# Kernel optimization log

Measured on AMD Instinct MI355X. Metric: run time of the kernel, lower is better.

## Reference

```python
import jax, jax.numpy as jnp
import numpy as np

D_IN = 4096
NUM_HEADS = 32
NUM_KV_GROUPS = 8
HEAD_DIM = D_IN // NUM_HEADS  # 128 (init overwrites head_dim)
GROUP_SIZE = NUM_HEADS // NUM_KV_GROUPS
SEQ = 2048
BATCH = 1
EPS = 1e-6


def layernorm(t, w, b):
    mu = jnp.mean(t, axis=-1, keepdims=True)
    var = jnp.var(t, axis=-1, keepdims=True)
    return (t - mu) * jax.lax.rsqrt(var + EPS) * w + b


def rope(t, cos, sin):
    # t: [B, H, S, D]; cos/sin: [S, D] broadcast over B, H
    half = t.shape[-1] // 2
    x1, x2 = t[..., :half], t[..., half:]
    rot = jnp.concatenate([-x2, x1], axis=-1)
    return t * cos + rot * sin


def setup_inputs() -> dict:
    key = jax.random.key(0)
    ks = jax.random.split(key, 10)
    x = jax.random.normal(ks[0], (BATCH, SEQ, D_IN), dtype=jnp.float32)
    mask = jnp.triu(jnp.ones((SEQ, SEQ), dtype=bool), k=1)  # True = masked (causal)
    # RoPE tables
    inv_freq = 1.0 / (10000.0 ** (np.arange(0, HEAD_DIM, 2, dtype=np.float32) / HEAD_DIM))
    pos = np.arange(SEQ, dtype=np.float32)
    ang = np.einsum('s,d->sd', pos, inv_freq)  # [S, D/2]
    ang = np.concatenate([ang, ang], axis=-1)  # [S, D]
    cos = jnp.asarray(np.cos(ang))
    sin = jnp.asarray(np.sin(ang))
    s = 0.02
    Wq = jax.random.normal(ks[1], (D_IN, NUM_HEADS * HEAD_DIM), dtype=jnp.float32) * s
    Wk = jax.random.normal(ks[2], (D_IN, NUM_KV_GROUPS * HEAD_DIM), dtype=jnp.float32) * s
    Wv = jax.random.normal(ks[3], (D_IN, NUM_KV_GROUPS * HEAD_DIM), dtype=jnp.float32) * s
    Wo = jax.random.normal(ks[4], (NUM_HEADS * HEAD_DIM, D_IN), dtype=jnp.float32) * s
    qn_w = jnp.ones((HEAD_DIM,), jnp.float32)
    qn_b = jnp.zeros((HEAD_DIM,), jnp.float32)
    kn_w = jnp.ones((HEAD_DIM,), jnp.float32)
    kn_b = jnp.zeros((HEAD_DIM,), jnp.float32)
    return {"x": x, "mask": mask, "cos": cos, "sin": sin, "Wq": Wq, "Wk": Wk,
            "Wv": Wv, "Wo": Wo, "qn_w": qn_w, "qn_b": qn_b, "kn_w": kn_w, "kn_b": kn_b}


def reference(x, mask, cos, sin, Wq, Wk, Wv, Wo, qn_w, qn_b, kn_w, kn_b):
    B, S, _ = x.shape
    q = (x @ Wq).reshape(B, S, NUM_HEADS, HEAD_DIM).transpose(0, 2, 1, 3)      # [B,H,S,D]
    k = (x @ Wk).reshape(B, S, NUM_KV_GROUPS, HEAD_DIM).transpose(0, 2, 1, 3)  # [B,G,S,D]
    v = (x @ Wv).reshape(B, S, NUM_KV_GROUPS, HEAD_DIM).transpose(0, 2, 1, 3)
    q = layernorm(q, qn_w, qn_b)
    k = layernorm(k, kn_w, kn_b)
    q = rope(q, cos, sin)
    k = rope(k, cos, sin)
    k = jnp.repeat(k, GROUP_SIZE, axis=1)  # [B,H,S,D]
    v = jnp.repeat(v, GROUP_SIZE, axis=1)
    scores = jnp.einsum('bhqd,bhkd->bhqk', q, k)
    scores = jnp.where(mask, -jnp.inf, scores)
    attn = jax.nn.softmax(scores / jnp.sqrt(jnp.float32(HEAD_DIM)), axis=-1)
    ctx = jnp.einsum('bhqk,bhkd->bhqd', attn, v)
    ctx = ctx.transpose(0, 2, 1, 3).reshape(B, S, NUM_HEADS * HEAD_DIM)
    return ctx @ Wo
```

## Files before the change

kernel.cpp:

```cpp
#include <hip/hip_runtime.h>
#include <stdint.h>

#define SQ   2048
#define DIN  4096
#define NH   32
#define NKV  8
#define HD   128
#define NQKV 6144

typedef float f32x4 __attribute__((ext_vector_type(4)));
typedef short bf16x8 __attribute__((ext_vector_type(8)));

__device__ __forceinline__ short f2bf(float f) {
  union { float f; uint32_t u; } v; v.f = f;
  uint32_t r = (v.u + 0x7FFFu + ((v.u >> 16) & 1u)) >> 16;
  return (short)r;
}

__device__ __forceinline__ void gl2lds(const void* g, void* l) {
  __builtin_amdgcn_global_load_lds(
      (const __attribute__((address_space(1))) void*)g,
      (__attribute__((address_space(3))) void*)l, 16, 0, 0);
}

__global__ void cvt_bf16(const float* __restrict__ src, short* __restrict__ dst, long n) {
  long i = ((long)blockIdx.x * blockDim.x + threadIdx.x) * 4;
  if (i + 3 < n) {
    float4 v = *(const float4*)(src + i);
    short o[4] = { f2bf(v.x), f2bf(v.y), f2bf(v.z), f2bf(v.w) };
    *(uint2*)(dst + i) = *(uint2*)o;
  }
}

__global__ __launch_bounds__(256) void transpose_cvt(const float* __restrict__ src, int ldS, long zS,
                                                     short* __restrict__ dst, int ldD, long zD) {
  __shared__ float tile[64][65];
  src += (long)blockIdx.z * zS;
  dst += (long)blockIdx.z * zD;
  int r0 = blockIdx.y * 64, c0 = blockIdx.x * 64;
  int tid = threadIdx.x;
#pragma unroll
  for (int i = 0; i < 16; ++i) {
    int idx = i * 256 + tid;
    int rr = idx >> 6, cc = idx & 63;
    tile[rr][cc] = src[(long)(r0 + rr) * ldS + c0 + cc];
  }
  __syncthreads();
#pragma unroll
  for (int i = 0; i < 16; ++i) {
    int idx = i * 256 + tid;
    int dr = idx >> 6, dc = idx & 63;
    dst[(long)(c0 + dr) * ldD + r0 + dc] = f2bf(tile[dc][dr]);
  }
}

#define ASZ   16384
#define BUFSZ 32768
#define MFMA(d, a, b) d = __builtin_amdgcn_mfma_f32_16x16x32_bf16(a, b, d, 0, 0, 0)

#define SA(t) { short* d = &lds[(((t) & 1) * BUFSZ) + dA]; const short* s = aS + (long)(t) * 64; \
                gl2lds(s, d); gl2lds(s + K8, d + 512); gl2lds(s + 2 * K8, d + 1024); gl2lds(s + 3 * K8, d + 1536); }
#define SB(t) { short* d = &lds[(((t) & 1) * BUFSZ) + dB]; const short* s = bS + (long)(t) * 64; \
                gl2lds(s, d); gl2lds(s + K8, d + 512); gl2lds(s + 2 * K8, d + 1024); gl2lds(s + 3 * K8, d + 1536); }

__global__ __launch_bounds__(512, 2) void gemm8p(const short* __restrict__ A, const short* __restrict__ Bt,
                                                 float* __restrict__ C, int M, int N, int K) {
  __shared__ __align__(16) short lds[2 * BUFSZ];
  int nwg = gridDim.x;
  int lin = ((int)blockIdx.x & 7) * (nwg >> 3) + ((int)blockIdx.x >> 3);
  int mt = M >> 8;
  int m0 = (lin % mt) << 8, n0 = (lin / mt) << 8;

  int tid = threadIdx.x;
  int w = tid >> 6, lane = tid & 63;
  int l16 = lane & 15, lq = lane >> 4;
  int wm = (w >> 2) << 7;
  int wn = (w & 3) << 6;

  int s7 = l16 & 7;
  int fo0 = ((lq ^ s7) << 3);
  int fo1 = (((lq + 4) ^ s7) << 3);
  int arow = (wm + l16) * 64;
  int brow = ASZ + (wn + l16) * 64;

  int srow = lane >> 3;
  int gch = (lane & 7) ^ srow;
  const short* aS = A + (long)(m0 + 32 * w + srow) * K + gch * 8;
  const short* bS = Bt + (long)(n0 + 32 * w + srow) * K + gch * 8;
  long K8 = 8L * K;
  int dA = (32 * w) * 64;
  int dB = ASZ + (32 * w) * 64;

  f32x4 acc[8][4] = {};
  const int KT = K >> 6;

  SA(0); SB(0);
  asm volatile("s_waitcnt vmcnt(0)" ::: "memory");
  __builtin_amdgcn_s_barrier();

  for (int t = 0; t < KT; ++t) {
    const short* buf = &lds[(t & 1) * BUFSZ];
    bool s1 = (t + 1 < KT);
    bf16x8 af[8], b0, b1;

#pragma unroll
    for (int i = 0; i < 8; ++i) af[i] = *(const bf16x8*)&buf[arow + i * 1024 + fo0];
    b0 = *(const bf16x8*)&buf[brow + fo0];
    b1 = *(const bf16x8*)&buf[brow + 1024 + fo0];
    if (s1) SA(t + 1);
    __builtin_amdgcn_s_barrier();
    asm volatile("s_waitcnt lgkmcnt(0)" ::: "memory");
    __builtin_amdgcn_s_setprio(1);
#pragma unroll
    for (int i = 0; i < 8; ++i) { MFMA(acc[i][0], af[i], b0); MFMA(acc[i][1], af[i], b1); }
    __builtin_amdgcn_s_setprio(0);
    __builtin_amdgcn_s_barrier();

    b0 = *(const bf16x8*)&buf[brow + 2048 + fo0];
    b1 = *(const bf16x8*)&buf[brow + 3072 + fo0];
    if (s1) SB(t + 1);
    __builtin_amdgcn_s_barrier();
    asm volatile("s_waitcnt lgkmcnt(0)" ::: "memory");
    __builtin_amdgcn_s_setprio(1);
#pragma unroll
    for (int i = 0; i < 8; ++i) { MFMA(acc[i][2], af[i], b0); MFMA(acc[i][3], af[i], b1); }
    __builtin_amdgcn_s_setprio(0);
    __builtin_amdgcn_s_barrier();

#pragma unroll
    for (int i = 0; i < 8; ++i) af[i] = *(const bf16x8*)&buf[arow + i * 1024 + fo1];
    b0 = *(const bf16x8*)&buf[brow + 2048 + fo1];
    b1 = *(const bf16x8*)&buf[brow + 3072 + fo1];
    __builtin_amdgcn_s_barrier();
    asm volatile("s_waitcnt lgkmcnt(0)" ::: "memory");
    __builtin_amdgcn_s_setprio(1);
#pragma unroll
    for (int i = 0; i < 8; ++i) { MFMA(acc[i][2], af[i], b0); MFMA(acc[i][3], af[i], b1); }
    __builtin_amdgcn_s_setprio(0);
    __builtin_amdgcn_s_barrier();

    b0 = *(const bf16x8*)&buf[brow + fo1];
    b1 = *(const bf16x8*)&buf[brow + 1024 + fo1];
    __builtin_amdgcn_s_barrier();
    asm volatile("s_waitcnt lgkmcnt(0)" ::: "memory");
    __builtin_amdgcn_s_setprio(1);
#pragma unroll
    for (int i = 0; i < 8; ++i) { MFMA(acc[i][0], af[i], b0); MFMA(acc[i][1], af[i], b1); }
    __builtin_amdgcn_s_setprio(0);
    if (s1) {
      asm volatile("s_waitcnt vmcnt(0)" ::: "memory");
      __builtin_amdgcn_s_barrier();
    }
  }

#pragma unroll
  for (int i = 0; i < 8; ++i)
#pragma unroll
    for (int j = 0; j < 4; ++j)
#pragma unroll
      for (int r = 0; r < 4; ++r)
        C[(long)(m0 + wm + i * 16 + lq * 4 + r) * N + n0 + wn + j * 16 + l16] = acc[i][j][r];
}

#define A3SZ 16384
#define T3SZ 24576

#define SA3(t) { short* d = &lds[((t) % 3) * T3SZ + dA]; const short* s = aS + (long)(t) * 64; \
                 gl2lds(s, d); gl2lds(s + K8, d + 512); gl2lds(s + 2 * K8, d + 1024); gl2lds(s + 3 * K8, d + 1536); }
#define SB3(t) { short* d = &lds[((t) % 3) * T3SZ + dB]; const short* s = bS + (long)(t) * 64; \
                 gl2lds(s, d); gl2lds(s + K8, d + 512); }

__global__ __launch_bounds__(512) void gemm3b(const short* __restrict__ A, const short* __restrict__ Bt,
                                              float* __restrict__ C, int M, int N, int K) {
  __shared__ __align__(16) short lds[3 * T3SZ];
  int nwg = gridDim.x;
  int lin = ((int)blockIdx.x & 7) * (nwg >> 3) + ((int)blockIdx.x >> 3);
  int mt = M >> 8;
  int m0 = (lin % mt) << 8, n0 = (lin / mt) << 7;

  int tid = threadIdx.x;
  int w = tid >> 6, lane = tid & 63;
  int l16 = lane & 15, lq = lane >> 4;
  int wm = (w >> 1) << 6;
  int wn = (w & 1) << 6;

  int s7 = l16 & 7;
  int fo0 = ((lq ^ s7) << 3);
  int fo1 = (((lq + 4) ^ s7) << 3);
  int arow = (wm + l16) * 64;
  int brow = A3SZ + (wn + l16) * 64;

  int srow = lane >> 3;
  int gch = (lane & 7) ^ srow;
  const short* aS = A + (long)(m0 + 32 * w + srow) * K + gch * 8;
  const short* bS = Bt + (long)(n0 + 16 * w + srow) * K + gch * 8;
  long K8 = 8L * K;
  int dA = w * 2048;
  int dB = A3SZ + w * 1024;

  f32x4 acc[4][4] = {};
  const int KT = K >> 6;

  SA3(0); SB3(0); SA3(1); SB3(1);
  asm volatile("s_waitcnt vmcnt(6)" ::: "memory");
  __builtin_amdgcn_s_barrier();

  for (int t = 0; t < KT; ++t) {
    const short* buf = &lds[(t % 3) * T3SZ];
    bool s2 = (t + 2 < KT);
    bf16x8 af[4], bfv[4];

#pragma unroll
    for (int i = 0; i < 4; ++i) af[i] = *(const bf16x8*)&buf[arow + i * 1024 + fo0];
#pragma unroll
    for (int j = 0; j < 4; ++j) bfv[j] = *(const bf16x8*)&buf[brow + j * 1024 + fo0];
    if (s2) SA3(t + 2);
    __builtin_amdgcn_s_barrier();
    asm volatile("s_waitcnt lgkmcnt(0)" ::: "memory");
    __builtin_amdgcn_s_setprio(1);
#pragma unroll
    for (int i = 0; i < 4; ++i)
#pragma unroll
      for (int j = 0; j < 4; ++j) MFMA(acc[i][j], af[i], bfv[j]);
    __builtin_amdgcn_s_setprio(0);
    __builtin_amdgcn_s_barrier();

#pragma unroll
    for (int i = 0; i < 4; ++i) af[i] = *(const bf16x8*)&buf[arow + i * 1024 + fo1];
#pragma unroll
    for (int j = 0; j < 4; ++j) bfv[j] = *(const bf16x8*)&buf[brow + j * 1024 + fo1];
    if (s2) SB3(t + 2);
    __builtin_amdgcn_s_barrier();
    asm volatile("s_waitcnt lgkmcnt(0)" ::: "memory");
    __builtin_amdgcn_s_setprio(1);
#pragma unroll
    for (int i = 0; i < 4; ++i)
#pragma unroll
      for (int j = 0; j < 4; ++j) MFMA(acc[i][j], af[i], bfv[j]);
    __builtin_amdgcn_s_setprio(0);
    if (t + 1 < KT) {
      if (s2) asm volatile("s_waitcnt vmcnt(6)" ::: "memory");
      else    asm volatile("s_waitcnt vmcnt(0)" ::: "memory");
      __builtin_amdgcn_s_barrier();
    }
  }

#pragma unroll
  for (int i = 0; i < 4; ++i)
#pragma unroll
    for (int j = 0; j < 4; ++j)
#pragma unroll
      for (int r = 0; r < 4; ++r)
        C[(long)(m0 + wm + i * 16 + lq * 4 + r) * N + n0 + wn + j * 16 + l16] = acc[i][j][r];
}

__global__ __launch_bounds__(64) void ln_rope(const float* __restrict__ qkv,
                                              const float* __restrict__ cosb, const float* __restrict__ sinb,
                                              const float* __restrict__ qw, const float* __restrict__ qb,
                                              const float* __restrict__ kw, const float* __restrict__ kb,
                                              short* __restrict__ qo, short* __restrict__ ko) {
  int s = blockIdx.x, slice = blockIdx.y, t = threadIdx.x;
  bool isq = slice < NH;
  int off = isq ? slice * HD : DIN + (slice - NH) * HD;
  const float* src = qkv + (long)s * NQKV + off;
  float v0 = src[t], v1 = src[t + 64];
  float sum = v0 + v1, ss = v0 * v0 + v1 * v1;
#pragma unroll
  for (int o = 1; o < 64; o <<= 1) { sum += __shfl_xor(sum, o); ss += __shfl_xor(ss, o); }
  float mu = sum * (1.f / 128.f);
  float var = ss * (1.f / 128.f) - mu * mu;
  float rstd = rsqrtf(var + 1e-6f);
  const float* w  = isq ? qw : kw;
  const float* bb = isq ? qb : kb;
  float n0 = (v0 - mu) * rstd * w[t]      + bb[t];
  float n1 = (v1 - mu) * rstd * w[t + 64] + bb[t + 64];
  float c0 = cosb[s * HD + t], c1 = cosb[s * HD + t + 64];
  float s0 = sinb[s * HD + t], s1 = sinb[s * HD + t + 64];
  float o0 = n0 * c0 - n1 * s0;
  float o1 = n1 * c1 + n0 * s1;
  short* dst = isq ? (qo + ((long)slice * SQ + s) * HD)
                   : (ko + ((long)(slice - NH) * SQ + s) * HD);
  dst[t] = f2bf(o0);
  dst[t + 64] = f2bf(o1);
}

__global__ __launch_bounds__(256) void attn(const short* __restrict__ q, const short* __restrict__ k,
                                            const short* __restrict__ vT, short* __restrict__ ctx) {
  int pair = blockIdx.x, h = blockIdx.y, g = h >> 2;
  int tid = threadIdx.x, w = tid >> 6, lane = tid & 63;
  int l16 = lane & 15, lq = lane >> 4;
  __shared__ __align__(16) short Ks[2][64 * 128];
  __shared__ __align__(16) short Vs[2][128 * 64];
  __shared__ __align__(16) short pbuf[4][16 * 72];
  const short* qh = q + (long)h * SQ * HD;
  const short* kg = k + (long)g * SQ * HD;
  const short* vg = vT + (long)g * HD * SQ;
  int kr = (w * 4) * 4 + (lane >> 4);
  int vrw = (w * 4) * 8 + (lane >> 3);
  const float sc = 0.08838834764831845f * 1.4426950408889634f;

  for (int st = 0; st < 2; ++st) {
    int qt = st ? (31 - pair) : pair;
    int qbase = qt * 64 + w * 16;
    bf16x8 aq[4];
#pragma unroll
    for (int kk = 0; kk < 4; ++kk)
      aq[kk] = *(const bf16x8*)&qh[(long)(qbase + l16) * HD + kk * 32 + lq * 8];
    float m_r[4], l_r[4];
    f32x4 acc[8] = {};
#pragma unroll
    for (int r = 0; r < 4; ++r) { m_r[r] = -__builtin_inff(); l_r[r] = 0.f; }

#pragma unroll
    for (int j = 0; j < 4; ++j) {
      int call = w * 4 + j;
      int r = kr + j * 4;
      int chk = (lane & 15) ^ (r & 15);
      gl2lds(&kg[(long)r * HD + chk * 8], &Ks[0][call * 512]);
      int rv = vrw + j * 8;
      int chv = (lane & 7) ^ (rv & 7);
      gl2lds(&vg[(long)rv * SQ + chv * 8], &Vs[0][call * 512]);
    }

    for (int kt = 0; kt <= qt; ++kt) {
      int cur = kt & 1;
      bool more = kt < qt;
      if (more) {
#pragma unroll
        for (int j = 0; j < 4; ++j) {
          int call = w * 4 + j;
          int r = kr + j * 4;
          int chk = (lane & 15) ^ (r & 15);
          gl2lds(&kg[(long)((kt + 1) * 64 + r) * HD + chk * 8], &Ks[cur ^ 1][call * 512]);
          int rv = vrw + j * 8;
          int chv = (lane & 7) ^ (rv & 7);
          gl2lds(&vg[(long)rv * SQ + (kt + 1) * 64 + chv * 8], &Vs[cur ^ 1][call * 512]);
        }
        asm volatile("s_waitcnt vmcnt(8)" ::: "memory");
      } else {
        asm volatile("s_waitcnt vmcnt(0)" ::: "memory");
      }
      __builtin_amdgcn_s_barrier();

      f32x4 s4[4];
#pragma unroll
      for (int b = 0; b < 4; ++b) s4[b] = (f32x4){0.f, 0.f, 0.f, 0.f};
#pragma unroll
      for (int b = 0; b < 4; ++b) {
        int krow = b * 16 + l16;
#pragma unroll
        for (int kk = 0; kk < 4; ++kk) {
          bf16x8 bk = *(const bf16x8*)&Ks[cur][krow * 128 + ((kk * 4 + lq) ^ (krow & 15)) * 8];
          s4[b] = __builtin_amdgcn_mfma_f32_16x16x32_bf16(aq[kk], bk, s4[b], 0, 0, 0);
        }
      }
      int qrow0 = qbase + lq * 4;
      if (kt == qt) {
#pragma unroll
        for (int b = 0; b < 4; ++b) {
          int key = kt * 64 + b * 16 + l16;
#pragma unroll
          for (int r = 0; r < 4; ++r) {
            float val = s4[b][r] * sc;
            s4[b][r] = (key > qrow0 + r) ? -__builtin_inff() : val;
          }
        }
      } else {
#pragma unroll
        for (int b = 0; b < 4; ++b)
#pragma unroll
          for (int r = 0; r < 4; ++r) s4[b][r] *= sc;
      }
      float mx4[4];
      bool defer = true;
#pragma unroll
      for (int r = 0; r < 4; ++r) {
        float mx = fmaxf(fmaxf(s4[0][r], s4[1][r]), fmaxf(s4[2][r], s4[3][r]));
#pragma unroll
        for (int o = 1; o < 16; o <<= 1) mx = fmaxf(mx, __shfl_xor(mx, o));
        mx4[r] = mx;
        defer = defer && (mx - m_r[r] <= 8.f);
      }
      if (!__all((int)defer)) {
#pragma unroll
        for (int r = 0; r < 4; ++r) {
          float mnew = fmaxf(m_r[r], mx4[r]);
          float alpha = exp2f(m_r[r] - mnew);
          l_r[r] *= alpha;
          m_r[r] = mnew;
#pragma unroll
          for (int n = 0; n < 8; ++n) acc[n][r] *= alpha;
        }
      }
      float p[4][4];
#pragma unroll
      for (int r = 0; r < 4; ++r) {
        float sum = 0.f;
#pragma unroll
        for (int b = 0; b < 4; ++b) { float pv = exp2f(s4[b][r] - m_r[r]); p[b][r] = pv; sum += pv; }
#pragma unroll
        for (int o = 1; o < 16; o <<= 1) sum += __shfl_xor(sum, o);
        l_r[r] += sum;
      }
#pragma unroll
      for (int b = 0; b < 4; ++b)
#pragma unroll
        for (int r = 0; r < 4; ++r)
          pbuf[w][(lq * 4 + r) * 72 + b * 16 + l16] = f2bf(p[b][r]);
#pragma unroll
      for (int kk = 0; kk < 2; ++kk) {
        bf16x8 pf = *(const bf16x8*)&pbuf[w][l16 * 72 + kk * 32 + lq * 8];
#pragma unroll
        for (int n = 0; n < 8; ++n) {
          int vrow = n * 16 + l16;
          bf16x8 vf = *(const bf16x8*)&Vs[cur][vrow * 64 + ((kk * 4 + lq) ^ (vrow & 7)) * 8];
          acc[n] = __builtin_amdgcn_mfma_f32_16x16x32_bf16(pf, vf, acc[n], 0, 0, 0);
        }
      }
      __builtin_amdgcn_s_barrier();
    }
#pragma unroll
    for (int n = 0; n < 8; ++n)
#pragma unroll
      for (int r = 0; r < 4; ++r) {
        int srow = qbase + lq * 4 + r;
        ctx[(long)srow * (NH * HD) + h * HD + n * 16 + l16] = f2bf(acc[n][r] / l_r[r]);
      }
  }
}

#define XB_OFF     0L
#define QR_OFF     0L
#define WQKVT_OFF  16777216L
#define KR_OFF     16777216L
#define VT_OFF     20971520L
#define CTX_OFF    25165824L
#define WOT_OFF    67108864L
#define QKV_OFF    100663296L

extern "C" void kernel_launch(void* const* d_in, const int* in_sizes, int n_in,
                              void* d_out, int out_size, void* d_ws, size_t ws_size,
                              hipStream_t stream) {
  const float* x    = (const float*)d_in[0];
  const float* cosb = (const float*)d_in[2];
  const float* sinb = (const float*)d_in[3];
  const float* Wq   = (const float*)d_in[4];
  const float* Wk   = (const float*)d_in[5];
  const float* Wv   = (const float*)d_in[6];
  const float* Wo   = (const float*)d_in[7];
  const float* qnw  = (const float*)d_in[8];
  const float* qnb  = (const float*)d_in[9];
  const float* knw  = (const float*)d_in[10];
  const float* knb  = (const float*)d_in[11];

  char* ws = (char*)d_ws;
  short* xb    = (short*)(ws + XB_OFF);
  short* qr    = (short*)(ws + QR_OFF);
  short* wqkvt = (short*)(ws + WQKVT_OFF);
  short* krp   = (short*)(ws + KR_OFF);
  short* vt    = (short*)(ws + VT_OFF);
  short* ctx   = (short*)(ws + CTX_OFF);
  short* wot   = (short*)(ws + WOT_OFF);
  float* qkv   = (float*)(ws + QKV_OFF);

  cvt_bf16<<<8192, 256, 0, stream>>>(x, xb, (long)SQ * DIN);
  transpose_cvt<<<dim3(64, 64, 1), 256, 0, stream>>>(Wq, 4096, 0L, wqkvt, 4096, 0L);
  transpose_cvt<<<dim3(16, 64, 1), 256, 0, stream>>>(Wk, 1024, 0L, wqkvt + (long)4096 * 4096, 4096, 0L);
  transpose_cvt<<<dim3(16, 64, 1), 256, 0, stream>>>(Wv, 1024, 0L, wqkvt + (long)5120 * 4096, 4096, 0L);
  transpose_cvt<<<dim3(64, 64, 1), 256, 0, stream>>>(Wo, 4096, 0L, wot, 4096, 0L);
  gemm8p<<<(SQ / 256) * (NQKV / 256), 512, 0, stream>>>(xb, wqkvt, qkv, SQ, NQKV, DIN);
  ln_rope<<<dim3(SQ, NH + NKV), 64, 0, stream>>>(qkv, cosb, sinb, qnw, qnb, knw, knb, qr, krp);
  transpose_cvt<<<dim3(2, 32, 8), 256, 0, stream>>>(qkv + 5120, NQKV, 128L, vt, SQ, (long)HD * SQ);
  attn<<<dim3(16, NH), 256, 0, stream>>>(qr, krp, vt, ctx);
  gemm3b<<<(SQ / 256) * (DIN / 128), 512, 0, stream>>>(ctx, wot, (float*)d_out, SQ, DIN, DIN);
}
```

Baseline: 546.8 us.

## Software-pipeline LDS fragment loads ahead of MFMA phases in GEMM main loop

Restructures the GEMM K-loop so the LDS fragments for each MFMA phase are loaded during the preceding phase, using double register sets (a0/a1, P/Q). The next tile's first fragments are prefetched at the end of each iteration. Explicit lgkmcnt waits and several barriers are dropped, and sched_barrier is used to keep the ordering. This aims to hide LDS latency behind MFMAs, at the cost of more VGPRs and more fragile synchronisation around buffer reuse.

```diff
diff --git a/kernel.cpp b/kernel.cpp
--- a/kernel.cpp
+++ b/kernel.cpp
@@ -92,65 +92,69 @@
   int dB = ASZ + (32 * w) * 64;
 
   f32x4 acc[8][4] = {};
+  bf16x8 a0[8], a1[8], P0, P1, Q0, Q1;
   const int KT = K >> 6;
 
   SA(0); SB(0);
   asm volatile("s_waitcnt vmcnt(0)" ::: "memory");
   __builtin_amdgcn_s_barrier();
+  {
+    const short* buf = &lds[0];
+#pragma unroll
+    for (int i = 0; i < 8; ++i) a0[i] = *(const bf16x8*)&buf[arow + i * 1024 + fo0];
+    P0 = *(const bf16x8*)&buf[brow + fo0];
+    P1 = *(const bf16x8*)&buf[brow + 1024 + fo0];
+  }
 
   for (int t = 0; t < KT; ++t) {
-    const short* buf = &lds[(t & 1) * BUFSZ];
+    const short* buf  = &lds[(t & 1) * BUFSZ];
+    const short* nbuf = &lds[((t + 1) & 1) * BUFSZ];
     bool s1 = (t + 1 < KT);
-    bf16x8 af[8], b0, b1;
-
-#pragma unroll
-    for (int i = 0; i < 8; ++i) af[i] = *(const bf16x8*)&buf[arow + i * 1024 + fo0];
-    b0 = *(const bf16x8*)&buf[brow + fo0];
-    b1 = *(const bf16x8*)&buf[brow + 1024 + fo0];
+
+    Q0 = *(const bf16x8*)&buf[brow + 2048 + fo0];
+    Q1 = *(const bf16x8*)&buf[brow + 3072 + fo0];
     if (s1) SA(t + 1);
-    __builtin_amdgcn_s_barrier();
-    asm volatile("s_waitcnt lgkmcnt(0)" ::: "memory");
-    __builtin_amdgcn_s_setprio(1);
-#pragma unroll
-    for (int i = 0; i < 8; ++i) { MFMA(acc[i][0], af[i], b0); MFMA(acc[i][1], af[i], b1); }
-    __builtin_amdgcn_s_setprio(0);
-    __builtin_amdgcn_s_barrier();
-
-    b0 = *(const bf16x8*)&buf[brow + 2048 + fo0];
-    b1 = *(const bf16x8*)&buf[brow + 3072 + fo0];
+    __builtin_amdgcn_sched_barrier(0);
+    __builtin_amdgcn_s_setprio(1);
+#pragma unroll
+    for (int i = 0; i < 8; ++i) { MFMA(acc[i][0], a0[i], P0); MFMA(acc[i][1], a0[i], P1); }
+    __builtin_amdgcn_s_setprio(0);
+    __builtin_amdgcn_s_barrier();
+
+#pragma unroll
+    for (int i = 0; i < 8; ++i) a1[i] = *(const bf16x8*)&buf[arow + i * 1024 + fo1];
+    P0 = *(const bf16x8*)&buf[brow + 2048 + fo1];
+    P1 = *(const bf16x8*)&buf[brow + 3072 + fo1];
     if (s1) SB(t + 1);
-    __builtin_amdgcn_s_barrier();
-    asm volatile("s_waitcnt lgkmcnt(0)" ::: "memory");
-    __builtin_amdgcn_s_setprio(1);
-#pragma unroll
-    for (int i = 0; i < 8; ++i) { MFMA(acc[i][2], af[i], b0); MFMA(acc[i][3], af[i], b1); }
-    __builtin_amdgcn_s_setprio(0);
-    __builtin_amdgcn_s_barrier();
-
-#pragma unroll
-    for (int i = 0; i < 8; ++i) af[i] = *(const bf16x8*)&buf[arow + i * 1024 + fo1];
-    b0 = *(const bf16x8*)&buf[brow + 2048 + fo1];
-    b1 = *(const bf16x8*)&buf[brow + 3072 + fo1];
-    __builtin_amdgcn_s_barrier();
-    asm volatile("s_waitcnt lgkmcnt(0)" ::: "memory");
-    __builtin_amdgcn_s_setprio(1);
-#pragma unroll
-    for (int i = 0; i < 8; ++i) { MFMA(acc[i][2], af[i], b0); MFMA(acc[i][3], af[i], b1); }
-    __builtin_amdgcn_s_setprio(0);
-    __builtin_amdgcn_s_barrier();
-
-    b0 = *(const bf16x8*)&buf[brow + fo1];
-    b1 = *(const bf16x8*)&buf[brow + 1024 + fo1];
-    __builtin_amdgcn_s_barrier();
-    asm volatile("s_waitcnt lgkmcnt(0)" ::: "memory");
-    __builtin_amdgcn_s_setprio(1);
-#pragma unroll
-    for (int i = 0; i < 8; ++i) { MFMA(acc[i][0], af[i], b0); MFMA(acc[i][1], af[i], b1); }
-    __builtin_amdgcn_s_setprio(0);
+    __builtin_amdgcn_sched_barrier(0);
+    __builtin_amdgcn_s_setprio(1);
+#pragma unroll
+    for (int i = 0; i < 8; ++i) { MFMA(acc[i][2], a0[i], Q0); MFMA(acc[i][3], a0[i], Q1); }
+    __builtin_amdgcn_s_setprio(0);
+    __builtin_amdgcn_s_barrier();
+
+    Q0 = *(const bf16x8*)&buf[brow + fo1];
+    Q1 = *(const bf16x8*)&buf[brow + 1024 + fo1];
+    __builtin_amdgcn_sched_barrier(0);
+    __builtin_amdgcn_s_setprio(1);
+#pragma unroll
+    for (int i = 0; i < 8; ++i) { MFMA(acc[i][2], a1[i], P0); MFMA(acc[i][3], a1[i], P1); }
+    __builtin_amdgcn_s_setprio(0);
+    if (s1) asm volatile("s_waitcnt vmcnt(0)" ::: "memory");
+    __builtin_amdgcn_s_barrier();
+
     if (s1) {
-      asm volatile("s_waitcnt vmcnt(0)" ::: "memory");
-      __builtin_amdgcn_s_barrier();
+#pragma unroll
+      for (int i = 0; i < 8; ++i) a0[i] = *(const bf16x8*)&nbuf[arow + i * 1024 + fo0];
+      P0 = *(const bf16x8*)&nbuf[brow + fo0];
+      P1 = *(const bf16x8*)&nbuf[brow + 1024 + fo0];
     }
+    __builtin_amdgcn_sched_barrier(0);
+    __builtin_amdgcn_s_setprio(1);
+#pragma unroll
+    for (int i = 0; i < 8; ++i) { MFMA(acc[i][0], a1[i], Q0); MFMA(acc[i][1], a1[i], Q1); }
+    __builtin_amdgcn_s_setprio(0);
+    __builtin_amdgcn_s_barrier();
   }
 
 #pragma unroll
```

After: 540.1 us. Within noise of the previous version (-1.2%).
